# Performance work log

Hardware: AMD Instinct MI355X
Metric: run time of the kernel (lower is better)

Reference implementation:

```python
import jax, jax.numpy as jnp
import numpy as np

B, S, HID = 1, 2048, 2048
H, KV, D = 16, 4, 128
N_REP = H // KV
WINDOW = 1024
THETA = 10000.0
EPS = 1e-6
SCALE = D ** -0.5


def setup_inputs() -> dict:
    key = jax.random.key(0)
    ks = jax.random.split(key, 10)
    s = 0.02
    return {
        "hidden_states": jax.random.normal(ks[0], (B, S, HID), jnp.float32),
        "Wq": jax.random.normal(ks[1], (HID, H * D), jnp.float32) * s,
        "bq": jnp.zeros((H * D,), jnp.float32),
        "Wk": jax.random.normal(ks[2], (HID, KV * D), jnp.float32) * s,
        "bk": jnp.zeros((KV * D,), jnp.float32),
        "Wv": jax.random.normal(ks[3], (HID, KV * D), jnp.float32) * s,
        "bv": jnp.zeros((KV * D,), jnp.float32),
        "Wo": jax.random.normal(ks[4], (H * D, HID), jnp.float32) * s,
        "memory_gate": jnp.zeros((1, H, 1, 1), jnp.float32),
    }


def _rope_tables(seq_len, dim, dtype):
    inv_freq = 1.0 / (THETA ** (jnp.arange(0, dim, 2, dtype=jnp.float32) / dim))
    t = jnp.arange(seq_len, dtype=jnp.float32)
    freqs = t[:, None] * inv_freq[None, :]          # [S, D/2]
    emb = jnp.concatenate([freqs, freqs], axis=-1)  # [S, D]
    return jnp.cos(emb).astype(dtype), jnp.sin(emb).astype(dtype)


def _rotate_half(x):
    x1, x2 = x[..., : x.shape[-1] // 2], x[..., x.shape[-1] // 2 :]
    return jnp.concatenate([-x2, x1], axis=-1)


def reference(hidden_states, Wq, bq, Wk, bk, Wv, bv, Wo, memory_gate):
    b, s, _ = hidden_states.shape
    q = (hidden_states @ Wq + bq).reshape(b, s, H, D).transpose(0, 2, 1, 3)   # [B,H,S,D]
    k = (hidden_states @ Wk + bk).reshape(b, s, KV, D).transpose(0, 2, 1, 3)  # [B,KV,S,D]
    v = (hidden_states @ Wv + bv).reshape(b, s, KV, D).transpose(0, 2, 1, 3)

    cos, sin = _rope_tables(s, D, q.dtype)  # [S,D]
    cos = cos[None, None]                   # [1,1,S,D]
    sin = sin[None, None]
    q_rot = q * cos + _rotate_half(q) * sin
    k_rot = k * cos + _rotate_half(k) * sin

    # GQA repeat of rotated K and raw V to H heads
    k_rep = jnp.repeat(k_rot, N_REP, axis=1)  # [B,H,S,D]
    v_rep = jnp.repeat(v, N_REP, axis=1)

    # sliding-window causal attention (seq_len > window path)
    scores = jnp.einsum("bhsd,bhtd->bhst", q_rot, k_rep) * SCALE
    row = jnp.arange(s)[:, None]
    col = jnp.arange(s)[None, :]
    mask = (col <= row) & (row - col < WINDOW)  # [S,S]
    scores = jnp.where(mask[None, None], scores, -jnp.inf)
    probs = jax.nn.softmax(scores.astype(jnp.float32), axis=-1).astype(q.dtype)
    local = jnp.einsum("bhst,bhtd->bhsd", probs, v_rep)

    # infini-memory retrieval: memory is reset before retrieve, so M=0, z=0
    sigma_q = jax.nn.elu(q) + 1.0                        # unrotated (NoPE) query
    M = jnp.zeros((b, H, D, D), q.dtype)
    z = jnp.zeros((b, H, D), q.dtype)
    num = jnp.einsum("bhsd,bhde->bhse", sigma_q, M)
    den = jnp.einsum("bhsd,bhd->bhs", sigma_q, z) + EPS
    global_out = num / den[..., None]                    # zeros, but faithful math

    gate = jax.nn.sigmoid(memory_gate)                   # [1,H,1,1]
    out = gate * global_out + (1.0 - gate) * local       # [B,H,S,D]
    out = out.transpose(0, 2, 1, 3).reshape(b, s, H * D)
    return out @ Wo
```

## Files before the change

### kernel.cpp

```cpp
#include <hip/hip_runtime.h>
#include <stdint.h>

typedef __attribute__((ext_vector_type(8))) short short8;
typedef __attribute__((ext_vector_type(4))) float f32x4;

#define S_LEN 2048
#define HID 2048
#define NH 16
#define NKV 4
#define DH 128
#define WINDOW 1024
#define SCALE 0.08838834764831845f

__device__ __forceinline__ unsigned short f2bf(float f) {
    unsigned int u = __float_as_uint(f);
    unsigned int r = (u + 0x7fffu + ((u >> 16) & 1u)) >> 16;
    return (unsigned short)r;
}

__device__ __forceinline__ void gload16(const void* g, void* l) {
    __builtin_amdgcn_global_load_lds((__attribute__((address_space(1))) void*)g,
                                     (__attribute__((address_space(3))) void*)l, 16, 0, 0);
}


__global__ __launch_bounds__(256) void cast4_kernel(const float* __restrict__ src,
                                                    unsigned short* __restrict__ dst, int n4) {
    int i = blockIdx.x * 256 + threadIdx.x;
    if (i < n4) {
        float4 v = ((const float4*)src)[i];
        ushort4 o;
        o.x = f2bf(v.x); o.y = f2bf(v.y); o.z = f2bf(v.z); o.w = f2bf(v.w);
        ((ushort4*)dst)[i] = o;
    }
}

__global__ __launch_bounds__(256) void build_bias_kernel(const float* __restrict__ bq,
                                                         const float* __restrict__ bk,
                                                         const float* __restrict__ bv,
                                                         float* __restrict__ cbias) {
    int i = blockIdx.x * 256 + threadIdx.x;
    if (i < 3072) {
        float v;
        if (i < 2048) v = bq[i];
        else if (i < 2560) v = bk[i - 2048];
        else v = bv[i - 2560];
        cbias[i] = v;
    }
}

__global__ __launch_bounds__(256) void transpose_cast_kernel(const float* __restrict__ src,
                                                             unsigned short* __restrict__ dst,
                                                             int N, int K, int rowoff) {
    __shared__ unsigned short t[32][33];
    int n0 = blockIdx.x * 32, k0 = blockIdx.y * 32;
    int c = threadIdx.x & 31, r8 = threadIdx.x >> 5;
#pragma unroll
    for (int i = 0; i < 4; i++) {
        int r = r8 + i * 8;
        t[r][c] = f2bf(src[(size_t)(k0 + r) * N + n0 + c]);
    }
    __syncthreads();
#pragma unroll
    for (int i = 0; i < 4; i++) {
        int r = r8 + i * 8;
        dst[(size_t)(rowoff + n0 + r) * K + k0 + c] = t[c][r];
    }
}


__global__ __launch_bounds__(256) void gemm_bf16(const unsigned short* __restrict__ A,
                                                 const unsigned short* __restrict__ Bt,
                                                 float* __restrict__ C,
                                                 const float* __restrict__ bias,
                                                 int M, int N, int K) {
    __shared__ unsigned short Al[2][128 * 32];
    __shared__ unsigned short Bl[2][128 * 32];
    const int tid = threadIdx.x;
    const int lane = tid & 63;
    const int w = tid >> 6;
    const int nbn = N >> 7;
    const int bm = blockIdx.x / nbn, bn = blockIdx.x % nbn;
    const int m0 = bm << 7, n0 = bn << 7;
    const int wr = w >> 1, wc = w & 1;

    const int lin0 = tid * 16;
    const int r0 = lin0 >> 6, b0 = lin0 & 63;
    const int lin1 = 4096 + tid * 16;
    const int r1 = lin1 >> 6, b1 = lin1 & 63;
    const size_t Kb = (size_t)K * 2;

    const char* Ab = (const char*)A + (size_t)m0 * Kb;
    const char* Bb = (const char*)Bt + (size_t)n0 * Kb;
    char* Al0 = (char*)&Al[0][0];
    char* Bl0 = (char*)&Bl[0][0];
    const int wb = w * 1024;

    auto stage = [&](int buf, int kt) {
        const char* Ak = Ab + kt * 64;
        const char* Bk = Bb + kt * 64;
        char* Ad = Al0 + buf * 8192;
        char* Bd = Bl0 + buf * 8192;
        gload16(Ak + (size_t)r0 * Kb + b0, Ad + wb);
        gload16(Ak + (size_t)r1 * Kb + b1, Ad + 4096 + wb);
        gload16(Bk + (size_t)r0 * Kb + b0, Bd + wb);
        gload16(Bk + (size_t)r1 * Kb + b1, Bd + 4096 + wb);
    };

    f32x4 acc[4][4] = {};
    const int NT = K >> 5;
    stage(0, 0);
    for (int kt = 0; kt < NT; ++kt) {
        __syncthreads();
        if (kt + 1 < NT) stage((kt + 1) & 1, kt + 1);
        const char* Ar = (const char*)&Al[kt & 1][0];
        const char* Br = (const char*)&Bl[kt & 1][0];
        const int ko = (lane >> 4) * 16;
        short8 af[4], bfr[4];
#pragma unroll
        for (int m = 0; m < 4; m++)
            af[m] = *(const short8*)(Ar + (wr * 64 + m * 16 + (lane & 15)) * 64 + ko);
#pragma unroll
        for (int n = 0; n < 4; n++)
            bfr[n] = *(const short8*)(Br + (wc * 64 + n * 16 + (lane & 15)) * 64 + ko);
#pragma unroll
        for (int m = 0; m < 4; m++)
#pragma unroll
            for (int n = 0; n < 4; n++)
                acc[m][n] = __builtin_amdgcn_mfma_f32_16x16x32_bf16(af[m], bfr[n], acc[m][n], 0, 0, 0);
        __syncthreads();
    }

#pragma unroll
    for (int m = 0; m < 4; m++) {
        const int row = m0 + wr * 64 + m * 16 + (lane >> 4) * 4;
#pragma unroll
        for (int n = 0; n < 4; n++) {
            const int col = n0 + wc * 64 + n * 16 + (lane & 15);
            const float badd = bias ? bias[col] : 0.f;
            float* Cp = C + (size_t)row * N + col;
#pragma unroll
            for (int r = 0; r < 4; r++)
                Cp[(size_t)r * N] = acc[m][n][r] + badd;
        }
    }
}

__global__ __launch_bounds__(256) void rope_kernel(const float* __restrict__ qkv,
                                                   unsigned short* __restrict__ Qr,
                                                   unsigned short* __restrict__ Kr,
                                                   unsigned short* __restrict__ Vt) {
    int s = blockIdx.x, tid = threadIdx.x;
    __shared__ float cs[64], sn[64];
    if (tid < 64) {
        float inv = __expf(-(float)tid * (logf(10000.f) / 64.f));
        float ang = (float)s * inv;
        float si, co;
        sincosf(ang, &si, &co);
        cs[tid] = co;
        sn[tid] = si;
    }
    __syncthreads();
    const float* row = qkv + (size_t)s * 3072;
#pragma unroll
    for (int it = 0; it < 8; ++it) {
        int j = tid + it * 256;
        int h = j >> 7, d = j & 127, f = d & 63;
        float x = row[j];
        float other = row[(j & ~127) + (d ^ 64)];
        float v = (d < 64) ? x * cs[f] - other * sn[f] : x * cs[f] + other * sn[f];
        Qr[((size_t)h * S_LEN + s) * 128 + d] = f2bf(v);
    }
#pragma unroll
    for (int it = 0; it < 2; ++it) {
        int j = tid + it * 256;
        int kvh = j >> 7, d = j & 127, f = d & 63;
        float x = row[2048 + j];
        float other = row[2048 + (j & ~127) + (d ^ 64)];
        float v = (d < 64) ? x * cs[f] - other * sn[f] : x * cs[f] + other * sn[f];
        Kr[((size_t)kvh * S_LEN + s) * 128 + d] = f2bf(v);
        float vv = row[2560 + j];
        Vt[((size_t)kvh * 128 + d) * S_LEN + s] = f2bf(vv);
    }
}


__global__ __launch_bounds__(256) void attn_kernel(const unsigned short* __restrict__ Qr,
                                                   const unsigned short* __restrict__ Kr,
                                                   const unsigned short* __restrict__ Vt,
                                                   const float* __restrict__ mg,
                                                   unsigned short* __restrict__ Ao) {
    __shared__ unsigned short Kl[2][64 * 128];
    __shared__ unsigned short Vl[2][128 * 64];
    __shared__ unsigned short Pl[4][16 * 64];
    const int tid = threadIdx.x, lane = tid & 63, w = tid >> 6;
    const int h = blockIdx.y, qt = blockIdx.x;
    const int kvh = h >> 2;
    const int q0 = qt * 64;

    const unsigned short* Qb =
        Qr + ((size_t)h * S_LEN + q0 + w * 16 + (lane & 15)) * 128 + (lane >> 4) * 8;
    short8 qf[4];
#pragma unroll
    for (int ks = 0; ks < 4; ++ks) qf[ks] = *(const short8*)(Qb + ks * 32);

    const float gate = 1.f / (1.f + __expf(-mg[h]));
    const float fac = 1.f - gate;

    float mrow[4] = {-INFINITY, -INFINITY, -INFINITY, -INFINITY};
    float lrow[4] = {0.f, 0.f, 0.f, 0.f};
    f32x4 o[8] = {};

    const char* Kg = (const char*)(Kr + (size_t)kvh * S_LEN * 128);
    const char* Vg = (const char*)(Vt + (size_t)kvh * 128 * S_LEN);
    char* Klb = (char*)&Kl[0][0];
    char* Vlb = (char*)&Vl[0][0];
    const int wb = w * 1024;

    auto stage = [&](int buf, int kt) {
        const int k0 = kt * 64;
#pragma unroll
        for (int iss = 0; iss < 4; ++iss) {
            int lin = iss * 4096 + tid * 16;
            int row = lin >> 8;
            int chunk = (lin >> 4) & 15;
            gload16(Kg + (size_t)(k0 + row) * 256 + ((chunk ^ (row & 7)) << 4),
                    Klb + buf * 16384 + iss * 4096 + wb);
            int d = lin >> 7;
            int vchunk = (lin >> 4) & 7;
            gload16(Vg + (size_t)d * (S_LEN * 2) + (size_t)k0 * 2 + ((vchunk ^ (d & 7)) << 4),
                    Vlb + buf * 16384 + iss * 4096 + wb);
        }
    };

    const int t0 = (q0 >= 1023) ? (q0 - 1023) >> 6 : 0;
    stage(0, t0);
    for (int kt = t0; kt <= qt; ++kt) {
        __syncthreads();
        if (kt < qt) stage((kt - t0 + 1) & 1, kt + 1);
        const int buf = (kt - t0) & 1;
        const int k0 = kt * 64;
        const char* Kb = Klb + buf * 16384;
        const char* Vb = Vlb + buf * 16384;

        f32x4 sc[4];
#pragma unroll
        for (int t = 0; t < 4; t++) {
            sc[t] = (f32x4){0.f, 0.f, 0.f, 0.f};
            const int krow = t * 16 + (lane & 15);
#pragma unroll
            for (int ks = 0; ks < 4; ks++) {
                const int chunk = ks * 4 + (lane >> 4);
                short8 kf = *(const short8*)(Kb + krow * 256 + ((chunk ^ (krow & 7)) << 4));
                sc[t] = __builtin_amdgcn_mfma_f32_16x16x32_bf16(qf[ks], kf, sc[t], 0, 0, 0);
            }
        }

        const int qrow_base = q0 + w * 16 + (lane >> 4) * 4;
        float alpha[4];
        float ps[4][4];
#pragma unroll
        for (int r = 0; r < 4; r++) {
            const int q = qrow_base + r;
            float mt = -INFINITY;
#pragma unroll
            for (int t = 0; t < 4; t++) {
                const int k = k0 + t * 16 + (lane & 15);
                const bool valid = (k <= q) && (q - k < WINDOW);
                float sv = valid ? sc[t][r] * SCALE : -INFINITY;
                ps[t][r] = sv;
                mt = fmaxf(mt, sv);
            }
#pragma unroll
            for (int off = 1; off < 16; off <<= 1) mt = fmaxf(mt, __shfl_xor(mt, off, 64));
            float mn = fmaxf(mrow[r], mt);
            alpha[r] = (mn == -INFINITY) ? 1.f : __expf(mrow[r] - mn);
            float ls = 0.f;
#pragma unroll
            for (int t = 0; t < 4; t++) {
                float p = (ps[t][r] == -INFINITY) ? 0.f : __expf(ps[t][r] - mn);
                ps[t][r] = p;
                ls += p;
            }
#pragma unroll
            for (int off = 1; off < 16; off <<= 1) ls += __shfl_xor(ls, off, 64);
            lrow[r] = lrow[r] * alpha[r] + ls;
            mrow[r] = mn;
        }

        char* Pw = (char*)&Pl[w][0];
#pragma unroll
        for (int r = 0; r < 4; r++) {
            const int row = (lane >> 4) * 4 + r;
#pragma unroll
            for (int t = 0; t < 4; t++) {
                const int col = t * 16 + (lane & 15);
                const int chunk = col >> 3;
                *(unsigned short*)(Pw + row * 128 + ((chunk ^ (row & 7)) << 4) + (col & 7) * 2) =
                    f2bf(ps[t][r]);
            }
        }
        asm volatile("s_waitcnt lgkmcnt(0)" ::: "memory");
        __builtin_amdgcn_sched_barrier(0);

#pragma unroll
        for (int n = 0; n < 8; n++)
#pragma unroll
            for (int r = 0; r < 4; r++) o[n][r] *= alpha[r];

#pragma unroll
        for (int n = 0; n < 8; n++) {
            const int d = n * 16 + (lane & 15);
#pragma unroll
            for (int ks = 0; ks < 2; ++ks) {
                const int chunk = ks * 4 + (lane >> 4);
                const int prow = lane & 15;
                short8 pa = *(const short8*)(Pw + prow * 128 + ((chunk ^ (prow & 7)) << 4));
                short8 vbf = *(const short8*)(Vb + d * 128 + ((chunk ^ (d & 7)) << 4));
                o[n] = __builtin_amdgcn_mfma_f32_16x16x32_bf16(pa, vbf, o[n], 0, 0, 0);
            }
        }
        __syncthreads();
    }

#pragma unroll
    for (int r = 0; r < 4; r++) {
        const int s = q0 + w * 16 + (lane >> 4) * 4 + r;
        const float inv = fac / lrow[r];
#pragma unroll
        for (int n = 0; n < 8; n++) {
            const int d = n * 16 + (lane & 15);
            Ao[(size_t)s * 2048 + h * 128 + d] = f2bf(o[n][r] * inv);
        }
    }
}


extern "C" void kernel_launch(void* const* d_in, const int* in_sizes, int n_in,
                              void* d_out, int out_size, void* d_ws, size_t ws_size,
                              hipStream_t stream) {
    const float* hs = (const float*)d_in[0];
    const float* Wq = (const float*)d_in[1];
    const float* bq = (const float*)d_in[2];
    const float* Wk = (const float*)d_in[3];
    const float* bk = (const float*)d_in[4];
    const float* Wv = (const float*)d_in[5];
    const float* bv = (const float*)d_in[6];
    const float* Wo = (const float*)d_in[7];
    const float* mg = (const float*)d_in[8];

    char* ws = (char*)d_ws;
    unsigned short* hsb   = (unsigned short*)(ws + 0);
    unsigned short* woT   = (unsigned short*)(ws + 0);
    unsigned short* wqkvT = (unsigned short*)(ws + 8388608);
    unsigned short* attnb = (unsigned short*)(ws + 8388608);
    float*          qkvf  = (float*)(ws + 20971520);
    unsigned short* Qrb   = (unsigned short*)(ws + 46137344);
    unsigned short* Krb   = (unsigned short*)(ws + 54525952);
    unsigned short* Vtb   = (unsigned short*)(ws + 56623104);
    float*          cbias = (float*)(ws + 58720256);

    cast4_kernel<<<4096, 256, 0, stream>>>(hs, hsb, 1048576);
    build_bias_kernel<<<12, 256, 0, stream>>>(bq, bk, bv, cbias);
    transpose_cast_kernel<<<dim3(64, 64), 256, 0, stream>>>(Wq, wqkvT, 2048, 2048, 0);
    transpose_cast_kernel<<<dim3(16, 64), 256, 0, stream>>>(Wk, wqkvT, 512, 2048, 2048);
    transpose_cast_kernel<<<dim3(16, 64), 256, 0, stream>>>(Wv, wqkvT, 512, 2048, 2560);

    gemm_bf16<<<16 * 24, 256, 0, stream>>>(hsb, wqkvT, qkvf, cbias, 2048, 3072, 2048);

    transpose_cast_kernel<<<dim3(64, 64), 256, 0, stream>>>(Wo, woT, 2048, 2048, 0);

    rope_kernel<<<2048, 256, 0, stream>>>(qkvf, Qrb, Krb, Vtb);

    attn_kernel<<<dim3(32, 16), 256, 0, stream>>>(Qrb, Krb, Vtb, mg, attnb);

    gemm_bf16<<<16 * 16, 256, 0, stream>>>(attnb, woT, (float*)d_out, nullptr, 2048, 2048, 2048);
}
```

Measured before the change: 280.9 us.

## Shrink GEMM N-tile, emit bf16 QKV, and read K/V directly from global in attention

The GEMM tile shrinks from 128x128 to 128x64 so more blocks are launched. The QKV projection now writes bf16 instead of fp32, which halves that intermediate's traffic, and the rope kernel reads bf16 and copies V through without a recast. The attention kernel drops its LDS double-buffered K/V staging and per-tile block barriers, loading K and V fragments straight from global memory and relying on cache reuse. The risks are uncoalesced, higher-latency global fragment loads in attention, and rounding the pre-RoPE Q/K to bf16 before rotation.

After: 346.5 us. +23.3%, slower.

```diff
diff --git a/kernel.cpp b/kernel.cpp
--- a/kernel.cpp
+++ b/kernel.cpp
@@ -16,6 +16,10 @@
     unsigned int u = __float_as_uint(f);
     unsigned int r = (u + 0x7fffu + ((u >> 16) & 1u)) >> 16;
     return (unsigned short)r;
+}
+
+__device__ __forceinline__ float bf2f(unsigned short u) {
+    return __uint_as_float((unsigned int)u << 16);
 }
 
 __device__ __forceinline__ void gload16(const void* g, void* l) {
@@ -69,19 +73,20 @@
 }
 
 
+template <bool BF16OUT>
 __global__ __launch_bounds__(256) void gemm_bf16(const unsigned short* __restrict__ A,
                                                  const unsigned short* __restrict__ Bt,
-                                                 float* __restrict__ C,
+                                                 void* __restrict__ Cv,
                                                  const float* __restrict__ bias,
                                                  int M, int N, int K) {
     __shared__ unsigned short Al[2][128 * 32];
-    __shared__ unsigned short Bl[2][128 * 32];
+    __shared__ unsigned short Bl[2][64 * 32];
     const int tid = threadIdx.x;
     const int lane = tid & 63;
     const int w = tid >> 6;
-    const int nbn = N >> 7;
+    const int nbn = N >> 6;
     const int bm = blockIdx.x / nbn, bn = blockIdx.x % nbn;
-    const int m0 = bm << 7, n0 = bn << 7;
+    const int m0 = bm << 7, n0 = bn << 6;
     const int wr = w >> 1, wc = w & 1;
 
     const int lin0 = tid * 16;
@@ -100,14 +105,13 @@
         const char* Ak = Ab + kt * 64;
         const char* Bk = Bb + kt * 64;
         char* Ad = Al0 + buf * 8192;
-        char* Bd = Bl0 + buf * 8192;
+        char* Bd = Bl0 + buf * 4096;
         gload16(Ak + (size_t)r0 * Kb + b0, Ad + wb);
         gload16(Ak + (size_t)r1 * Kb + b1, Ad + 4096 + wb);
         gload16(Bk + (size_t)r0 * Kb + b0, Bd + wb);
-        gload16(Bk + (size_t)r1 * Kb + b1, Bd + 4096 + wb);
     };
 
-    f32x4 acc[4][4] = {};
+    f32x4 acc[4][2] = {};
     const int NT = K >> 5;
     stage(0, 0);
     for (int kt = 0; kt < NT; ++kt) {
@@ -116,17 +120,17 @@
         const char* Ar = (const char*)&Al[kt & 1][0];
         const char* Br = (const char*)&Bl[kt & 1][0];
         const int ko = (lane >> 4) * 16;
-        short8 af[4], bfr[4];
+        short8 af[4], bfr[2];
 #pragma unroll
         for (int m = 0; m < 4; m++)
             af[m] = *(const short8*)(Ar + (wr * 64 + m * 16 + (lane & 15)) * 64 + ko);
 #pragma unroll
-        for (int n = 0; n < 4; n++)
-            bfr[n] = *(const short8*)(Br + (wc * 64 + n * 16 + (lane & 15)) * 64 + ko);
+        for (int n = 0; n < 2; n++)
+            bfr[n] = *(const short8*)(Br + (wc * 32 + n * 16 + (lane & 15)) * 64 + ko);
 #pragma unroll
         for (int m = 0; m < 4; m++)
 #pragma unroll
-            for (int n = 0; n < 4; n++)
+            for (int n = 0; n < 2; n++)
                 acc[m][n] = __builtin_amdgcn_mfma_f32_16x16x32_bf16(af[m], bfr[n], acc[m][n], 0, 0, 0);
         __syncthreads();
     }
@@ -135,18 +139,22 @@
     for (int m = 0; m < 4; m++) {
         const int row = m0 + wr * 64 + m * 16 + (lane >> 4) * 4;
 #pragma unroll
-        for (int n = 0; n < 4; n++) {
-            const int col = n0 + wc * 64 + n * 16 + (lane & 15);
+        for (int n = 0; n < 2; n++) {
+            const int col = n0 + wc * 32 + n * 16 + (lane & 15);
             const float badd = bias ? bias[col] : 0.f;
-            float* Cp = C + (size_t)row * N + col;
-#pragma unroll
-            for (int r = 0; r < 4; r++)
-                Cp[(size_t)r * N] = acc[m][n][r] + badd;
-        }
-    }
-}
-
-__global__ __launch_bounds__(256) void rope_kernel(const float* __restrict__ qkv,
+#pragma unroll
+            for (int r = 0; r < 4; r++) {
+                const float v = acc[m][n][r] + badd;
+                if constexpr (BF16OUT)
+                    ((unsigned short*)Cv)[(size_t)(row + r) * N + col] = f2bf(v);
+                else
+                    ((float*)Cv)[(size_t)(row + r) * N + col] = v;
+            }
+        }
+    }
+}
+
+__global__ __launch_bounds__(256) void rope_kernel(const unsigned short* __restrict__ qkv,
                                                    unsigned short* __restrict__ Qr,
                                                    unsigned short* __restrict__ Kr,
                                                    unsigned short* __restrict__ Vt) {
@@ -161,13 +169,13 @@
         sn[tid] = si;
     }
     __syncthreads();
-    const float* row = qkv + (size_t)s * 3072;
+    const unsigned short* row = qkv + (size_t)s * 3072;
 #pragma unroll
     for (int it = 0; it < 8; ++it) {
         int j = tid + it * 256;
         int h = j >> 7, d = j & 127, f = d & 63;
-        float x = row[j];
-        float other = row[(j & ~127) + (d ^ 64)];
+        float x = bf2f(row[j]);
+        float other = bf2f(row[(j & ~127) + (d ^ 64)]);
         float v = (d < 64) ? x * cs[f] - other * sn[f] : x * cs[f] + other * sn[f];
         Qr[((size_t)h * S_LEN + s) * 128 + d] = f2bf(v);
     }
@@ -175,12 +183,11 @@
     for (int it = 0; it < 2; ++it) {
         int j = tid + it * 256;
         int kvh = j >> 7, d = j & 127, f = d & 63;
-        float x = row[2048 + j];
-        float other = row[2048 + (j & ~127) + (d ^ 64)];
+        float x = bf2f(row[2048 + j]);
+        float other = bf2f(row[2048 + (j & ~127) + (d ^ 64)]);
         float v = (d < 64) ? x * cs[f] - other * sn[f] : x * cs[f] + other * sn[f];
         Kr[((size_t)kvh * S_LEN + s) * 128 + d] = f2bf(v);
-        float vv = row[2560 + j];
-        Vt[((size_t)kvh * 128 + d) * S_LEN + s] = f2bf(vv);
+        Vt[((size_t)kvh * 128 + d) * S_LEN + s] = row[2560 + j];
     }
 }
 
@@ -190,16 +197,15 @@
                                                    const unsigned short* __restrict__ Vt,
                                                    const float* __restrict__ mg,
                                                    unsigned short* __restrict__ Ao) {
-    __shared__ unsigned short Kl[2][64 * 128];
-    __shared__ unsigned short Vl[2][128 * 64];
     __shared__ unsigned short Pl[4][16 * 64];
     const int tid = threadIdx.x, lane = tid & 63, w = tid >> 6;
     const int h = blockIdx.y, qt = blockIdx.x;
     const int kvh = h >> 2;
     const int q0 = qt * 64;
+    const int lo = lane & 15, hi = lane >> 4;
 
     const unsigned short* Qb =
-        Qr + ((size_t)h * S_LEN + q0 + w * 16 + (lane & 15)) * 128 + (lane >> 4) * 8;
+        Qr + ((size_t)h * S_LEN + q0 + w * 16 + lo) * 128 + hi * 8;
     short8 qf[4];
 #pragma unroll
     for (int ks = 0; ks < 4; ++ks) qf[ks] = *(const short8*)(Qb + ks * 32);
@@ -213,50 +219,25 @@
 
     const char* Kg = (const char*)(Kr + (size_t)kvh * S_LEN * 128);
     const char* Vg = (const char*)(Vt + (size_t)kvh * 128 * S_LEN);
-    char* Klb = (char*)&Kl[0][0];
-    char* Vlb = (char*)&Vl[0][0];
-    const int wb = w * 1024;
-
-    auto stage = [&](int buf, int kt) {
+    char* Pw = (char*)&Pl[w][0];
+
+    const int t0 = (q0 >= 1023) ? (q0 - 1023) >> 6 : 0;
+    for (int kt = t0; kt <= qt; ++kt) {
         const int k0 = kt * 64;
-#pragma unroll
-        for (int iss = 0; iss < 4; ++iss) {
-            int lin = iss * 4096 + tid * 16;
-            int row = lin >> 8;
-            int chunk = (lin >> 4) & 15;
-            gload16(Kg + (size_t)(k0 + row) * 256 + ((chunk ^ (row & 7)) << 4),
-                    Klb + buf * 16384 + iss * 4096 + wb);
-            int d = lin >> 7;
-            int vchunk = (lin >> 4) & 7;
-            gload16(Vg + (size_t)d * (S_LEN * 2) + (size_t)k0 * 2 + ((vchunk ^ (d & 7)) << 4),
-                    Vlb + buf * 16384 + iss * 4096 + wb);
-        }
-    };
-
-    const int t0 = (q0 >= 1023) ? (q0 - 1023) >> 6 : 0;
-    stage(0, t0);
-    for (int kt = t0; kt <= qt; ++kt) {
-        __syncthreads();
-        if (kt < qt) stage((kt - t0 + 1) & 1, kt + 1);
-        const int buf = (kt - t0) & 1;
-        const int k0 = kt * 64;
-        const char* Kb = Klb + buf * 16384;
-        const char* Vb = Vlb + buf * 16384;
 
         f32x4 sc[4];
 #pragma unroll
         for (int t = 0; t < 4; t++) {
             sc[t] = (f32x4){0.f, 0.f, 0.f, 0.f};
-            const int krow = t * 16 + (lane & 15);
+            const size_t krow = (size_t)(k0 + t * 16 + lo);
 #pragma unroll
             for (int ks = 0; ks < 4; ks++) {
-                const int chunk = ks * 4 + (lane >> 4);
-                short8 kf = *(const short8*)(Kb + krow * 256 + ((chunk ^ (krow & 7)) << 4));
+                short8 kf = *(const short8*)(Kg + krow * 256 + (ks * 4 + hi) * 16);
                 sc[t] = __builtin_amdgcn_mfma_f32_16x16x32_bf16(qf[ks], kf, sc[t], 0, 0, 0);
             }
         }
 
-        const int qrow_base = q0 + w * 16 + (lane >> 4) * 4;
+        const int qrow_base = q0 + w * 16 + hi * 4;
         float alpha[4];
         float ps[4][4];
 #pragma unroll
@@ -265,7 +246,7 @@
             float mt = -INFINITY;
 #pragma unroll
             for (int t = 0; t < 4; t++) {
-                const int k = k0 + t * 16 + (lane & 15);
+                const int k = k0 + t * 16 + lo;
                 const bool valid = (k <= q) && (q - k < WINDOW);
                 float sv = valid ? sc[t][r] * SCALE : -INFINITY;
                 ps[t][r] = sv;
@@ -288,15 +269,14 @@
             mrow[r] = mn;
         }
 
-        char* Pw = (char*)&Pl[w][0];
 #pragma unroll
         for (int r = 0; r < 4; r++) {
-            const int row = (lane >> 4) * 4 + r;
+            const int prow = hi * 4 + r;
 #pragma unroll
             for (int t = 0; t < 4; t++) {
-                const int col = t * 16 + (lane & 15);
+                const int col = t * 16 + lo;
                 const int chunk = col >> 3;
-                *(unsigned short*)(Pw + row * 128 + ((chunk ^ (row & 7)) << 4) + (col & 7) * 2) =
+                *(unsigned short*)(Pw + prow * 128 + ((chunk ^ (prow & 7)) << 4) + (col & 7) * 2) =
                     f2bf(ps[t][r]);
             }
         }
@@ -310,26 +290,26 @@
 
 #pragma unroll
         for (int n = 0; n < 8; n++) {
-            const int d = n * 16 + (lane & 15);
+            const int d = n * 16 + lo;
 #pragma unroll
             for (int ks = 0; ks < 2; ++ks) {
-                const int chunk = ks * 4 + (lane >> 4);
-                const int prow = lane & 15;
+                const int chunk = ks * 4 + hi;
+                const int prow = lo;
                 short8 pa = *(const short8*)(Pw + prow * 128 + ((chunk ^ (prow & 7)) << 4));
-                short8 vbf = *(const short8*)(Vb + d * 128 + ((chunk ^ (d & 7)) << 4));
+                short8 vbf = *(const short8*)(Vg + (size_t)d * (S_LEN * 2) +
+                                              (size_t)(k0 + ks * 32 + hi * 8) * 2);
                 o[n] = __builtin_amdgcn_mfma_f32_16x16x32_bf16(pa, vbf, o[n], 0, 0, 0);
             }
         }
-        __syncthreads();
     }
 
 #pragma unroll
     for (int r = 0; r < 4; r++) {
-        const int s = q0 + w * 16 + (lane >> 4) * 4 + r;
+        const int s = q0 + w * 16 + hi * 4 + r;
         const float inv = fac / lrow[r];
 #pragma unroll
         for (int n = 0; n < 8; n++) {
-            const int d = n * 16 + (lane & 15);
+            const int d = n * 16 + lo;
             Ao[(size_t)s * 2048 + h * 128 + d] = f2bf(o[n][r] * inv);
         }
     }
@@ -354,11 +334,11 @@
     unsigned short* woT   = (unsigned short*)(ws + 0);
     unsigned short* wqkvT = (unsigned short*)(ws + 8388608);
     unsigned short* attnb = (unsigned short*)(ws + 8388608);
-    float*          qkvf  = (float*)(ws + 20971520);
-    unsigned short* Qrb   = (unsigned short*)(ws + 46137344);
-    unsigned short* Krb   = (unsigned short*)(ws + 54525952);
-    unsigned short* Vtb   = (unsigned short*)(ws + 56623104);
-    float*          cbias = (float*)(ws + 58720256);
+    unsigned short* qkvb  = (unsigned short*)(ws + 20971520);
+    unsigned short* Qrb   = (unsigned short*)(ws + 33554432);
+    unsigned short* Krb   = (unsigned short*)(ws + 41943040);
+    unsigned short* Vtb   = (unsigned short*)(ws + 44040192);
+    float*          cbias = (float*)(ws + 46137344);
 
     cast4_kernel<<<4096, 256, 0, stream>>>(hs, hsb, 1048576);
     build_bias_kernel<<<12, 256, 0, stream>>>(bq, bk, bv, cbias);
@@ -366,13 +346,13 @@
     transpose_cast_kernel<<<dim3(16, 64), 256, 0, stream>>>(Wk, wqkvT, 512, 2048, 2048);
     transpose_cast_kernel<<<dim3(16, 64), 256, 0, stream>>>(Wv, wqkvT, 512, 2048, 2560);
 
-    gemm_bf16<<<16 * 24, 256, 0, stream>>>(hsb, wqkvT, qkvf, cbias, 2048, 3072, 2048);
+    gemm_bf16<true><<<16 * 48, 256, 0, stream>>>(hsb, wqkvT, qkvb, cbias, 2048, 3072, 2048);
 
     transpose_cast_kernel<<<dim3(64, 64), 256, 0, stream>>>(Wo, woT, 2048, 2048, 0);
 
-    rope_kernel<<<2048, 256, 0, stream>>>(qkvf, Qrb, Krb, Vtb);
+    rope_kernel<<<2048, 256, 0, stream>>>(qkvb, Qrb, Krb, Vtb);
 
     attn_kernel<<<dim3(32, 16), 256, 0, stream>>>(Qrb, Krb, Vtb, mg, attnb);
 
-    gemm_bf16<<<16 * 16, 256, 0, stream>>>(attnb, woT, (float*)d_out, nullptr, 2048, 2048, 2048);
-}
+    gemm_bf16<false><<<16 * 32, 256, 0, stream>>>(attnb, woT, (float*)d_out, nullptr, 2048, 2048, 2048);
+}
```

## Split-K GEMMs with atomic accumulation and lazy-rescale attention softmax

Applied to the files above, without the earlier changes.

The two GEMMs become split-K kernels (2-way for QKV, 4-way for output) that accumulate into buffers zeroed beforehand with float atomics. This raises block counts on the 256-CU device, which the original 384 and 256 block grids underfill. The attention kernel skips masking for fully valid tiles, rescales the running max only when it rises by more than a threshold, hoists the P fragment loads, and raises wave priority around the MFMA sections. The costs are extra zeroing kernels, atomic traffic, nondeterministic summation order, and larger exponent ranges in bf16 P values from the lazy rescale.

Measured after the change: 332.1 us. +18.2%, slower.

```diff
diff --git a/kernel.cpp b/kernel.cpp
--- a/kernel.cpp
+++ b/kernel.cpp
@@ -49,6 +49,12 @@
     }
 }
 
+__global__ __launch_bounds__(256) void zero_kernel(float4* __restrict__ p, int n4) {
+    int i = blockIdx.x * 256 + threadIdx.x;
+    int stride = gridDim.x * 256;
+    for (; i < n4; i += stride) p[i] = (float4){0.f, 0.f, 0.f, 0.f};
+}
+
 __global__ __launch_bounds__(256) void transpose_cast_kernel(const float* __restrict__ src,
                                                              unsigned short* __restrict__ dst,
                                                              int N, int K, int rowoff) {
@@ -69,11 +75,11 @@
 }
 
 
-__global__ __launch_bounds__(256) void gemm_bf16(const unsigned short* __restrict__ A,
-                                                 const unsigned short* __restrict__ Bt,
-                                                 float* __restrict__ C,
-                                                 const float* __restrict__ bias,
-                                                 int M, int N, int K) {
+__global__ __launch_bounds__(256) void gemm_sk(const unsigned short* __restrict__ A,
+                                               const unsigned short* __restrict__ Bt,
+                                               float* __restrict__ C,
+                                               const float* __restrict__ bias,
+                                               int M, int N, int K, int split) {
     __shared__ unsigned short Al[2][128 * 32];
     __shared__ unsigned short Bl[2][128 * 32];
     const int tid = threadIdx.x;
@@ -83,6 +89,8 @@
     const int bm = blockIdx.x / nbn, bn = blockIdx.x % nbn;
     const int m0 = bm << 7, n0 = bn << 7;
     const int wr = w >> 1, wc = w & 1;
+    const int Ksub = K / split;
+    const int kbase = blockIdx.y * Ksub;
 
     const int lin0 = tid * 16;
     const int r0 = lin0 >> 6, b0 = lin0 & 63;
@@ -90,8 +98,8 @@
     const int r1 = lin1 >> 6, b1 = lin1 & 63;
     const size_t Kb = (size_t)K * 2;
 
-    const char* Ab = (const char*)A + (size_t)m0 * Kb;
-    const char* Bb = (const char*)Bt + (size_t)n0 * Kb;
+    const char* Ab = (const char*)A + (size_t)m0 * Kb + (size_t)kbase * 2;
+    const char* Bb = (const char*)Bt + (size_t)n0 * Kb + (size_t)kbase * 2;
     char* Al0 = (char*)&Al[0][0];
     char* Bl0 = (char*)&Bl[0][0];
     const int wb = w * 1024;
@@ -108,7 +116,7 @@
     };
 
     f32x4 acc[4][4] = {};
-    const int NT = K >> 5;
+    const int NT = Ksub >> 5;
     stage(0, 0);
     for (int kt = 0; kt < NT; ++kt) {
         __syncthreads();
@@ -123,25 +131,28 @@
 #pragma unroll
         for (int n = 0; n < 4; n++)
             bfr[n] = *(const short8*)(Br + (wc * 64 + n * 16 + (lane & 15)) * 64 + ko);
+        __builtin_amdgcn_s_setprio(1);
 #pragma unroll
         for (int m = 0; m < 4; m++)
 #pragma unroll
             for (int n = 0; n < 4; n++)
                 acc[m][n] = __builtin_amdgcn_mfma_f32_16x16x32_bf16(af[m], bfr[n], acc[m][n], 0, 0, 0);
+        __builtin_amdgcn_s_setprio(0);
         __syncthreads();
     }
 
+    const bool addb = (bias != nullptr) && (blockIdx.y == 0);
 #pragma unroll
     for (int m = 0; m < 4; m++) {
         const int row = m0 + wr * 64 + m * 16 + (lane >> 4) * 4;
 #pragma unroll
         for (int n = 0; n < 4; n++) {
             const int col = n0 + wc * 64 + n * 16 + (lane & 15);
-            const float badd = bias ? bias[col] : 0.f;
+            const float badd = addb ? bias[col] : 0.f;
             float* Cp = C + (size_t)row * N + col;
 #pragma unroll
             for (int r = 0; r < 4; r++)
-                Cp[(size_t)r * N] = acc[m][n][r] + badd;
+                unsafeAtomicAdd(Cp + (size_t)r * N, acc[m][n][r] + badd);
         }
     }
 }
@@ -197,9 +208,10 @@
     const int h = blockIdx.y, qt = blockIdx.x;
     const int kvh = h >> 2;
     const int q0 = qt * 64;
+    const int lo = lane & 15, hi = lane >> 4;
 
     const unsigned short* Qb =
-        Qr + ((size_t)h * S_LEN + q0 + w * 16 + (lane & 15)) * 128 + (lane >> 4) * 8;
+        Qr + ((size_t)h * S_LEN + q0 + w * 16 + lo) * 128 + hi * 8;
     short8 qf[4];
 #pragma unroll
     for (int ks = 0; ks < 4; ++ks) qf[ks] = *(const short8*)(Qb + ks * 32);
@@ -233,6 +245,7 @@
         }
     };
 
+    const int qmin = q0 + w * 16;
     const int t0 = (q0 >= 1023) ? (q0 - 1023) >> 6 : 0;
     stage(0, t0);
     for (int kt = t0; kt <= qt; ++kt) {
@@ -244,92 +257,128 @@
         const char* Vb = Vlb + buf * 16384;
 
         f32x4 sc[4];
+        __builtin_amdgcn_s_setprio(1);
 #pragma unroll
         for (int t = 0; t < 4; t++) {
             sc[t] = (f32x4){0.f, 0.f, 0.f, 0.f};
-            const int krow = t * 16 + (lane & 15);
+            const int krow = t * 16 + lo;
 #pragma unroll
             for (int ks = 0; ks < 4; ks++) {
-                const int chunk = ks * 4 + (lane >> 4);
+                const int chunk = ks * 4 + hi;
                 short8 kf = *(const short8*)(Kb + krow * 256 + ((chunk ^ (krow & 7)) << 4));
                 sc[t] = __builtin_amdgcn_mfma_f32_16x16x32_bf16(qf[ks], kf, sc[t], 0, 0, 0);
             }
         }
-
-        const int qrow_base = q0 + w * 16 + (lane >> 4) * 4;
+        __builtin_amdgcn_s_setprio(0);
+
+        const bool full = (k0 + 63 <= qmin) && (k0 >= qmin + 15 - (WINDOW - 1));
+        float ps[4][4];
+        float mt[4];
+        if (full) {
+#pragma unroll
+            for (int r = 0; r < 4; r++) {
+                float m0v = -INFINITY;
+#pragma unroll
+                for (int t = 0; t < 4; t++) {
+                    float sv = sc[t][r] * SCALE;
+                    ps[t][r] = sv;
+                    m0v = fmaxf(m0v, sv);
+                }
+                mt[r] = m0v;
+            }
+        } else {
+#pragma unroll
+            for (int r = 0; r < 4; r++) {
+                const int q = qmin + hi * 4 + r;
+                float m0v = -INFINITY;
+#pragma unroll
+                for (int t = 0; t < 4; t++) {
+                    const int k = k0 + t * 16 + lo;
+                    const bool valid = (k <= q) && (q - k < WINDOW);
+                    float sv = valid ? sc[t][r] * SCALE : -INFINITY;
+                    ps[t][r] = sv;
+                    m0v = fmaxf(m0v, sv);
+                }
+                mt[r] = m0v;
+            }
+        }
+
         float alpha[4];
-        float ps[4][4];
+        bool need = false;
 #pragma unroll
         for (int r = 0; r < 4; r++) {
-            const int q = qrow_base + r;
-            float mt = -INFINITY;
+#pragma unroll
+            for (int off = 1; off < 16; off <<= 1) mt[r] = fmaxf(mt[r], __shfl_xor(mt[r], off, 64));
+            const float mo = mrow[r];
+            const float mn = (mt[r] > mo + 8.f) ? mt[r] : mo;
+            const bool resc = (mn != mo);
+            alpha[r] = resc ? __expf(mo - mn) : 1.f;
+            need = need || resc;
+            mrow[r] = mn;
+            const float mn_e = (mn == -INFINITY) ? 0.f : mn;
+            float ls = 0.f;
 #pragma unroll
             for (int t = 0; t < 4; t++) {
-                const int k = k0 + t * 16 + (lane & 15);
-                const bool valid = (k <= q) && (q - k < WINDOW);
-                float sv = valid ? sc[t][r] * SCALE : -INFINITY;
-                ps[t][r] = sv;
-                mt = fmaxf(mt, sv);
-            }
-#pragma unroll
-            for (int off = 1; off < 16; off <<= 1) mt = fmaxf(mt, __shfl_xor(mt, off, 64));
-            float mn = fmaxf(mrow[r], mt);
-            alpha[r] = (mn == -INFINITY) ? 1.f : __expf(mrow[r] - mn);
-            float ls = 0.f;
-#pragma unroll
-            for (int t = 0; t < 4; t++) {
-                float p = (ps[t][r] == -INFINITY) ? 0.f : __expf(ps[t][r] - mn);
+                float p = __expf(ps[t][r] - mn_e);
                 ps[t][r] = p;
                 ls += p;
             }
 #pragma unroll
             for (int off = 1; off < 16; off <<= 1) ls += __shfl_xor(ls, off, 64);
             lrow[r] = lrow[r] * alpha[r] + ls;
-            mrow[r] = mn;
         }
 
         char* Pw = (char*)&Pl[w][0];
 #pragma unroll
         for (int r = 0; r < 4; r++) {
-            const int row = (lane >> 4) * 4 + r;
+            const int prow = hi * 4 + r;
 #pragma unroll
             for (int t = 0; t < 4; t++) {
-                const int col = t * 16 + (lane & 15);
+                const int col = t * 16 + lo;
                 const int chunk = col >> 3;
-                *(unsigned short*)(Pw + row * 128 + ((chunk ^ (row & 7)) << 4) + (col & 7) * 2) =
+                *(unsigned short*)(Pw + prow * 128 + ((chunk ^ (prow & 7)) << 4) + (col & 7) * 2) =
                     f2bf(ps[t][r]);
             }
         }
         asm volatile("s_waitcnt lgkmcnt(0)" ::: "memory");
         __builtin_amdgcn_sched_barrier(0);
 
-#pragma unroll
-        for (int n = 0; n < 8; n++)
-#pragma unroll
-            for (int r = 0; r < 4; r++) o[n][r] *= alpha[r];
-
+        if (__any(need)) {
+#pragma unroll
+            for (int n = 0; n < 8; n++)
+#pragma unroll
+                for (int r = 0; r < 4; r++) o[n][r] *= alpha[r];
+        }
+
+        short8 pa[2];
+#pragma unroll
+        for (int ks = 0; ks < 2; ++ks) {
+            const int chunk = ks * 4 + hi;
+            pa[ks] = *(const short8*)(Pw + lo * 128 + ((chunk ^ (lo & 7)) << 4));
+        }
+
+        __builtin_amdgcn_s_setprio(1);
 #pragma unroll
         for (int n = 0; n < 8; n++) {
-            const int d = n * 16 + (lane & 15);
+            const int d = n * 16 + lo;
 #pragma unroll
             for (int ks = 0; ks < 2; ++ks) {
-                const int chunk = ks * 4 + (lane >> 4);
-                const int prow = lane & 15;
-                short8 pa = *(const short8*)(Pw + prow * 128 + ((chunk ^ (prow & 7)) << 4));
+                const int chunk = ks * 4 + hi;
                 short8 vbf = *(const short8*)(Vb + d * 128 + ((chunk ^ (d & 7)) << 4));
-                o[n] = __builtin_amdgcn_mfma_f32_16x16x32_bf16(pa, vbf, o[n], 0, 0, 0);
-            }
-        }
+                o[n] = __builtin_amdgcn_mfma_f32_16x16x32_bf16(pa[ks], vbf, o[n], 0, 0, 0);
+            }
+        }
+        __builtin_amdgcn_s_setprio(0);
         __syncthreads();
     }
 
 #pragma unroll
     for (int r = 0; r < 4; r++) {
-        const int s = q0 + w * 16 + (lane >> 4) * 4 + r;
+        const int s = q0 + w * 16 + hi * 4 + r;
         const float inv = fac / lrow[r];
 #pragma unroll
         for (int n = 0; n < 8; n++) {
-            const int d = n * 16 + (lane & 15);
+            const int d = n * 16 + lo;
             Ao[(size_t)s * 2048 + h * 128 + d] = f2bf(o[n][r] * inv);
         }
     }
@@ -365,8 +414,9 @@
     transpose_cast_kernel<<<dim3(64, 64), 256, 0, stream>>>(Wq, wqkvT, 2048, 2048, 0);
     transpose_cast_kernel<<<dim3(16, 64), 256, 0, stream>>>(Wk, wqkvT, 512, 2048, 2048);
     transpose_cast_kernel<<<dim3(16, 64), 256, 0, stream>>>(Wv, wqkvT, 512, 2048, 2560);
-
-    gemm_bf16<<<16 * 24, 256, 0, stream>>>(hsb, wqkvT, qkvf, cbias, 2048, 3072, 2048);
+    zero_kernel<<<2048, 256, 0, stream>>>((float4*)qkvf, 1572864);
+
+    gemm_sk<<<dim3(16 * 24, 2), 256, 0, stream>>>(hsb, wqkvT, qkvf, cbias, 2048, 3072, 2048, 2);
 
     transpose_cast_kernel<<<dim3(64, 64), 256, 0, stream>>>(Wo, woT, 2048, 2048, 0);
 
@@ -374,5 +424,6 @@
 
     attn_kernel<<<dim3(32, 16), 256, 0, stream>>>(Qrb, Krb, Vtb, mg, attnb);
 
-    gemm_bf16<<<16 * 16, 256, 0, stream>>>(attnb, woT, (float*)d_out, nullptr, 2048, 2048, 2048);
-}
+    zero_kernel<<<2048, 256, 0, stream>>>((float4*)d_out, 1048576);
+    gemm_sk<<<dim3(16 * 16, 4), 256, 0, stream>>>(attnb, woT, (float*)d_out, nullptr, 2048, 2048, 2048, 4);
+}
```
